# Kernel optimization log

Measured on AMD Instinct MI355X. Metric: run time of the kernel, lower is better.

The kernel has to match this reference:

```python
import jax, jax.numpy as jnp
import numpy as np
from jax import lax

B, CIN, COUT, H, W = 4, 256, 256, 64, 64
K = 3  # kernel size
PAD = 1
STRIDE = 1


def setup_inputs() -> dict:
    key = jax.random.key(0)
    k1, k2, k3, k4 = jax.random.split(key, 4)
    x = jax.random.normal(k1, (B, CIN, H, W), dtype=jnp.float32)
    # small offset weights so learned offsets are modest (original init is zeros)
    offset_w = jax.random.normal(k2, (3 * K * K, CIN, K, K), dtype=jnp.float32) * 0.01
    offset_b = jax.random.normal(k3, (3 * K * K,), dtype=jnp.float32) * 0.01
    dcn_w = jax.random.normal(k4, (COUT, CIN, K, K), dtype=jnp.float32) * (1.0 / np.sqrt(CIN * K * K))
    return {"x": x, "offset_w": offset_w, "offset_b": offset_b, "dcn_w": dcn_w}


def _dcnv2(x, offset_w, offset_b, dcn_w):
    b, c, h, w = x.shape
    kk = K * K
    # offset conv (standard 3x3, stride 1, pad 1)
    o = lax.conv_general_dilated(
        x, offset_w, (STRIDE, STRIDE), ((PAD, PAD), (PAD, PAD)),
        dimension_numbers=("NCHW", "OIHW", "NCHW"))
    o = o + offset_b[None, :, None, None]
    ho, wo = o.shape[2], o.shape[3]
    off = o[:, : 2 * kk].reshape(b, kk, 2, ho, wo)  # pairs are (dy, dx)
    dy, dx = off[:, :, 0], off[:, :, 1]             # [b,kk,ho,wo]
    mask = jax.nn.sigmoid(o[:, 2 * kk:])            # [b,kk,ho,wo]

    ki, kj = jnp.meshgrid(jnp.arange(K), jnp.arange(K), indexing="ij")
    ki = ki.reshape(kk).astype(jnp.float32)
    kj = kj.reshape(kk).astype(jnp.float32)
    base_y = (jnp.arange(ho, dtype=jnp.float32) * STRIDE - PAD)[None, None, :, None] + ki[None, :, None, None]
    base_x = (jnp.arange(wo, dtype=jnp.float32) * STRIDE - PAD)[None, None, None, :] + kj[None, :, None, None]
    py = base_y + dy  # [b,kk,ho,wo] sampling y
    px = base_x + dx  # sampling x

    y0 = jnp.floor(py)
    x0 = jnp.floor(px)
    wy = py - y0  # bilinear fractional weights
    wx = px - x0
    y0i = y0.astype(jnp.int32)
    x0i = x0.astype(jnp.int32)

    xT = x.transpose(0, 2, 3, 1)  # [b,h,w,c] for channel-last gathers
    bidx = jnp.arange(b)[:, None, None, None]

    def gather(yi, xi):
        # zero padding outside the image
        valid = (yi >= 0) & (yi < h) & (xi >= 0) & (xi < w)
        yc = jnp.clip(yi, 0, h - 1)
        xc = jnp.clip(xi, 0, w - 1)
        v = xT[bidx, yc, xc]  # [b,kk,ho,wo,c]
        return v * valid[..., None].astype(x.dtype)

    g00 = gather(y0i, x0i)
    g01 = gather(y0i, x0i + 1)
    g10 = gather(y0i + 1, x0i)
    g11 = gather(y0i + 1, x0i + 1)

    wy_ = wy[..., None]
    wx_ = wx[..., None]
    sampled = (g00 * (1 - wy_) * (1 - wx_) + g01 * (1 - wy_) * wx_
               + g10 * wy_ * (1 - wx_) + g11 * wy_ * wx_)
    sampled = sampled * mask[..., None]  # modulation

    wk = dcn_w.reshape(dcn_w.shape[0], c, kk)  # [o,c,kk]
    return jnp.einsum("bkhwc,ock->bohw", sampled, wk)


def reference(x, offset_w, offset_b, dcn_w):
    return _dcnv2(x, offset_w, offset_b, dcn_w)
```

## Files before the change

### kernel.cpp

```cpp
#include <hip/hip_runtime.h>
#include <hip/hip_bf16.h>
#include <stdint.h>
#include <math.h>

#define KDIM 2304

typedef __attribute__((ext_vector_type(8))) short bf16x8;
typedef __attribute__((ext_vector_type(4))) float f32x4;

__device__ inline unsigned short f2bf(float f) {
  union { float f; unsigned int u; } v; v.f = f;
  unsigned int u = v.u;
  unsigned int r = (u + 0x7FFFu + ((u >> 16) & 1u)) >> 16;
  return (unsigned short)r;
}
__device__ inline float bf2f(unsigned short h) {
  union { unsigned int u; float f; } v; v.u = ((unsigned int)h) << 16;
  return v.f;
}

__device__ inline void gl2lds16(const void* g, void* l) {
  __builtin_amdgcn_global_load_lds((const __attribute__((address_space(1))) void*)g,
                                   (__attribute__((address_space(3))) void*)l,
                                   16, 0, 0);
}

#define GLOAD16(dst, ptr) \
  asm volatile("global_load_dwordx4 %0, %1, off" : "=v"(dst) : "v"(ptr))

__global__ __launch_bounds__(256) void k_prep(const float* __restrict__ x,
                                              unsigned short* __restrict__ xTb,
                                              const float* __restrict__ dcn_w,
                                              const float* __restrict__ offset_w,
                                              unsigned short* __restrict__ Wpk,
                                              unsigned short* __restrict__ Wob,
                                              unsigned short* __restrict__ zp) {
  __shared__ float tile[32][65];
  int bx = (int)blockIdx.x;
  int t = threadIdx.x;
  if (bx < 2048) {
    int pt = bx & 127, ct = (bx >> 7) & 3, b = bx >> 9;
    int p0 = pt * 32, c0 = ct * 64;
    const float* xb = x + ((size_t)b << 20);
#pragma unroll
    for (int i = 0; i < 2; ++i) {
      int idx = t + i * 256;
      int c = idx >> 3, pq = idx & 7;
      float4 v = *(const float4*)(xb + ((size_t)(c0 + c) << 12) + p0 + pq * 4);
      tile[pq * 4 + 0][c] = v.x;
      tile[pq * 4 + 1][c] = v.y;
      tile[pq * 4 + 2][c] = v.z;
      tile[pq * 4 + 3][c] = v.w;
    }
    __syncthreads();
    unsigned short* ob = xTb + ((size_t)b << 20);
#pragma unroll
    for (int i = 0; i < 2; ++i) {
      int idx = t + i * 256;
      int p = idx >> 4, cg = idx & 15;
      ushort4 o;
      o.x = f2bf(tile[p][cg * 4 + 0]);
      o.y = f2bf(tile[p][cg * 4 + 1]);
      o.z = f2bf(tile[p][cg * 4 + 2]);
      o.w = f2bf(tile[p][cg * 4 + 3]);
      *(ushort4*)(ob + (((size_t)(p0 + p)) << 8) + c0 + cg * 4) = o;
    }
  } else {
    int gid = (bx - 2048) * 256 + t;
    const int N1 = 72 * 8192;
    const int N2 = 32 * KDIM;
    if (gid < N1) {
      int j = gid & 7;
      int lane = (gid >> 3) & 63;
      int mb = (gid >> 9) & 15;
      int kc = gid >> 13;
      int row = mb * 16 + (lane & 15);
      int gk = kc * 32 + ((lane >> 4) << 3) + j;
      int c = gk & 255, kidx = gk >> 8;
      Wpk[gid] = f2bf(dcn_w[((size_t)(row * 256 + c)) * 9 + kidx]);
    } else if (gid < N1 + N2) {
      int g = gid - N1;
      int ch = g / KDIM, k = g % KDIM;
      int kidx = k >> 8, c = k & 255;
      Wob[g] = (ch < 27) ? f2bf(offset_w[((size_t)(ch * 256 + c)) * 9 + kidx])
                         : (unsigned short)0;
    } else if (gid < N1 + N2 + 128) {
      zp[gid - N1 - N2] = 0;
    }
  }
}

__global__ __launch_bounds__(256) void k_offs(const unsigned short* __restrict__ xTb,
                                              const unsigned short* __restrict__ Wob,
                                              const unsigned short* __restrict__ zp,
                                              const float* __restrict__ offb,
                                              float* __restrict__ SW) {
  __shared__ unsigned short As[4][32 * 32];
  __shared__ unsigned short Bs[4][32 * 32];
  __shared__ float Os[32][33];
  int t = threadIdx.x;
  int wv = t >> 6, lane = t & 63;
  int bid = (int)blockIdx.x;
  int swz = (bid & 7) * 64 + (bid >> 3);
  int n0 = swz * 32;

  int r0 = (t >> 2) & 31, coff = (t & 3) * 8;
  int rowA = n0 + r0;
  int b_ = rowA >> 12, hw = rowA & 4095, h = hw >> 6, w = hw & 63;
  int rB = ((t - 128) >> 2) & 31;

  f32x4 acc = {};

  auto stage = [&](int kt) {
    int buf = kt & 3;
    int k0 = kt * 32;
    int kidx = k0 >> 8, c0 = k0 & 255;
    if (t < 128) {
      int di = kidx / 3 - 1, dj = kidx % 3 - 1;
      int y = h + di, xx = w + dj;
      const unsigned short* g = (y >= 0 && y < 64 && xx >= 0 && xx < 64)
          ? xTb + (((((size_t)b_) << 12) + (y << 6) + xx) << 8) + c0 + coff
          : zp;
      gl2lds16(g, (char*)As[buf] + wv * 1024);
    } else {
      const unsigned short* gB = Wob + (size_t)rB * KDIM + k0 + coff;
      gl2lds16(gB, (char*)Bs[buf] + (wv - 2) * 1024);
    }
  };

  stage(0); stage(1); stage(2);

  int mf = wv & 1, nf = wv >> 1;
  for (int kt = 0; kt < 72; ++kt) {
    if (kt <= 69)      asm volatile("s_waitcnt vmcnt(2)" ::: "memory");
    else if (kt == 70) asm volatile("s_waitcnt vmcnt(1)" ::: "memory");
    else               asm volatile("s_waitcnt vmcnt(0)" ::: "memory");
    asm volatile("s_barrier" ::: "memory");
    if (kt + 3 < 72) stage(kt + 3);
    int buf = kt & 3;
    bf16x8 aF = *(const bf16x8*)(As[buf] + (mf * 16 + (lane & 15)) * 32 + (lane >> 4) * 8);
    bf16x8 bF = *(const bf16x8*)(Bs[buf] + (nf * 16 + (lane & 15)) * 32 + (lane >> 4) * 8);
    acc = __builtin_amdgcn_mfma_f32_16x16x32_bf16(aF, bF, acc, 0, 0, 0);
  }

  int quad = lane >> 4, cl = lane & 15;
#pragma unroll
  for (int r = 0; r < 4; ++r)
    Os[mf * 16 + quad * 4 + r][nf * 16 + cl] = acc[r];
  __syncthreads();

  for (int item = t; item < 288; item += 256) {
    int bl = item & 31, k = item >> 5;
    int bhw = n0 + bl;
    int h_ = (bhw >> 6) & 63, w_ = bhw & 63;
    float dy = Os[bl][2 * k]     + offb[2 * k];
    float dx = Os[bl][2 * k + 1] + offb[2 * k + 1];
    float mv = Os[bl][18 + k]    + offb[18 + k];
    float mask = 1.0f / (1.0f + expf(-mv));

    float py = (float)(h_ - 1 + k / 3) + dy;
    float px = (float)(w_ - 1 + k % 3) + dx;
    float y0f = floorf(py), x0f = floorf(px);
    float wy = py - y0f, wx = px - x0f;
    int y0 = (int)y0f, x0 = (int)x0f;
    int y1 = y0 + 1, x1 = x0 + 1;

    float vy0 = (y0 >= 0 && y0 < 64) ? 1.f : 0.f;
    float vy1 = (y1 >= 0 && y1 < 64) ? 1.f : 0.f;
    float vx0 = (x0 >= 0 && x0 < 64) ? 1.f : 0.f;
    float vx1 = (x1 >= 0 && x1 < 64) ? 1.f : 0.f;
    int y0c = min(max(y0, 0), 63), y1c = min(max(y1, 0), 63);
    int x0c = min(max(x0, 0), 63), x1c = min(max(x1, 0), 63);

    float4 wv4;
    wv4.x = (1.f - wy) * (1.f - wx) * vy0 * vx0 * mask;
    wv4.y = (1.f - wy) * wx * vy0 * vx1 * mask;
    wv4.z = wy * (1.f - wx) * vy1 * vx0 * mask;
    wv4.w = wy * wx * vy1 * vx1 * mask;
    uint4 ov;
    ov.x = (unsigned)(((y0c << 6) + x0c) << 8);
    ov.y = (unsigned)(((y0c << 6) + x1c) << 8);
    ov.z = (unsigned)(((y1c << 6) + x0c) << 8);
    ov.w = (unsigned)(((y1c << 6) + x1c) << 8);

    float* p = SW + (size_t)(k * 16384 + bhw) * 8;
    *(float4*)p = wv4;
    *(uint4*)(p + 4) = ov;
  }
}

#define PHASE(PH, Q, AF, BUF, WB, WM)                                          \
  do {                                                                         \
    if (((PH) & 3) == 0) {                                                     \
      int g_ = (PH) >> 2;                                                      \
      wv4 = *(const float4*)(SWL + (size_t)(g_ * 128 + r * 2) * 4);            \
      ov  = *(const uint4*)(SWL + (size_t)(g_ * 128 + r * 2 + 1) * 4);         \
    } else if (((PH) & 3) == 2 && (PH) < 32) {                                 \
      ov  = *(const uint4*)(SWL + (size_t)((((PH) >> 2) + 1) * 128 + r * 2 + 1) * 4); \
    }                                                                          \
    asm volatile("s_waitcnt vmcnt(" #WB ")" ::: "memory");                     \
    __builtin_amdgcn_sched_barrier(0);                                         \
    float s_[8];                                                               \
    _Pragma("unroll")                                                          \
    for (int j_ = 0; j_ < 8; ++j_)                                             \
      s_[j_] = wv4.x * bf2f((unsigned short)Q[0][j_]) +                        \
               wv4.y * bf2f((unsigned short)Q[1][j_]) +                        \
               wv4.z * bf2f((unsigned short)Q[2][j_]) +                        \
               wv4.w * bf2f((unsigned short)Q[3][j_]);                         \
    union { __hip_bfloat162 h2[4]; bf16x8 v; } pk_;                            \
    pk_.h2[0] = __float22bfloat162_rn(make_float2(s_[0], s_[1]));              \
    pk_.h2[1] = __float22bfloat162_rn(make_float2(s_[2], s_[3]));              \
    pk_.h2[2] = __float22bfloat162_rn(make_float2(s_[4], s_[5]));              \
    pk_.h2[3] = __float22bfloat162_rn(make_float2(s_[6], s_[7]));              \
    *(bf16x8*)(&Bs[BUF][s_th][bsw]) = pk_.v;                                   \
    if ((PH) < 34) {                                                           \
      int kn0_ = 2 * (PH) + 4;                                                 \
      unsigned c_ = (unsigned)((((kn0_ & 7) + s_th) << 5) + gg * 8);           \
      GLOAD16(Q[0], xb + ov.x + c_);                                           \
      GLOAD16(Q[1], xb + ov.y + c_);                                           \
      GLOAD16(Q[2], xb + ov.z + c_);                                           \
      GLOAD16(Q[3], xb + ov.w + c_);                                           \
    }                                                                          \
    asm volatile("s_waitcnt vmcnt(" #WM ") lgkmcnt(0)\n\ts_barrier" ::: "memory"); \
    __builtin_amdgcn_sched_barrier(0);                                         \
    _Pragma("unroll")                                                          \
    for (int s2_ = 0; s2_ < 2; ++s2_) {                                        \
      bf16x8 bF0_ = *(const bf16x8*)(                                          \
          &Bs[BUF][s2_][(wn * 32 + (lane & 15)) * 56 + (lane >> 4) * 8]);      \
      bf16x8 bF1_ = *(const bf16x8*)(                                          \
          &Bs[BUF][s2_][(wn * 32 + 16 + (lane & 15)) * 56 + (lane >> 4) * 8]); \
      _Pragma("unroll")                                                        \
      for (int i_ = 0; i_ < 4; ++i_) {                                         \
        acc[i_][0] = __builtin_amdgcn_mfma_f32_16x16x32_bf16(                  \
            AF[s2_ * 4 + i_], bF0_, acc[i_][0], 0, 0, 0);                      \
        acc[i_][1] = __builtin_amdgcn_mfma_f32_16x16x32_bf16(                  \
            AF[s2_ * 4 + i_], bF1_, acc[i_][1], 0, 0, 0);                      \
      }                                                                        \
    }                                                                          \
    if ((PH) < 34) {                                                           \
      _Pragma("unroll")                                                        \
      for (int i_ = 0; i_ < 8; ++i_) {                                         \
        const unsigned short* ap_ =                                            \
            wpBase + ((size_t)((2 * (PH) + 4 + (i_ >> 2)) * 16 + (i_ & 3))) * 512; \
        GLOAD16(AF[i_], ap_);                                                  \
      }                                                                        \
    }                                                                          \
  } while (0)

__global__ __launch_bounds__(512, 2) void k_fused(const unsigned short* __restrict__ Wpk,
                                                  const unsigned short* __restrict__ xTb,
                                                  const float* __restrict__ SW,
                                                  float* __restrict__ out) {
  __shared__ __align__(16) unsigned short Bs[2][2][64 * 56];
  __shared__ __align__(16) float SWL[1152 * 4];
  int t = threadIdx.x;
  int wv = t >> 6, lane = t & 63;
  int wm = wv & 3, wn = wv >> 2;
  int bid = (int)blockIdx.x;
  int swz = (bid & 7) * 32 + (bid >> 3);
  int n0 = swz * 64;
  int b  = n0 >> 12;
  const unsigned short* xb = xTb + ((size_t)b << 20);

  int r = t >> 3;
  int u = t & 7;
  int s_th = u & 1, gg = u >> 1;
  int bsw = r * 56 + gg * 8;

  const unsigned short* wpBase = Wpk + ((size_t)(wm * 4 * 64 + lane)) * 8;

  f32x4 acc[4][2] = {};

  {
#pragma unroll
    for (int i = 0; i < 3; ++i) {
      int hs = t + i * 512;
      if (hs < 1152) {
        int grp = hs >> 7, row = (hs >> 1) & 63, hh = hs & 1;
        const float* src = SW + ((size_t)(grp * 16384 + n0 + row)) * 8 + hh * 4;
        char* dstbase = (char*)SWL + ((size_t)((t & ~63) + i * 512)) * 16;
        gl2lds16(src, dstbase);
      }
    }
  }
  asm volatile("s_waitcnt vmcnt(0)" ::: "memory");
  __builtin_amdgcn_s_barrier();

  float4 wv4; uint4 ov;
  wv4 = *(const float4*)(SWL + (size_t)(r * 2) * 4);
  ov  = *(const uint4*)(SWL + (size_t)(r * 2 + 1) * 4);

  bf16x8 qA[4], qB[4];
  bf16x8 aFA[8], aFB[8];

  {
    unsigned cA = (unsigned)((s_th << 5) + gg * 8);
    GLOAD16(qA[0], xb + ov.x + cA);
    GLOAD16(qA[1], xb + ov.y + cA);
    GLOAD16(qA[2], xb + ov.z + cA);
    GLOAD16(qA[3], xb + ov.w + cA);
#pragma unroll
    for (int i = 0; i < 8; ++i) {
      const unsigned short* ap = wpBase + ((size_t)(((i >> 2)) * 16 + (i & 3))) * 512;
      GLOAD16(aFA[i], ap);
    }
    unsigned cB = (unsigned)(((2 + s_th) << 5) + gg * 8);
    GLOAD16(qB[0], xb + ov.x + cB);
    GLOAD16(qB[1], xb + ov.y + cB);
    GLOAD16(qB[2], xb + ov.z + cB);
    GLOAD16(qB[3], xb + ov.w + cB);
#pragma unroll
    for (int i = 0; i < 8; ++i) {
      const unsigned short* ap = wpBase + ((size_t)((2 + (i >> 2)) * 16 + (i & 3))) * 512;
      GLOAD16(aFB[i], ap);
    }
  }

  for (int ph = 0; ph < 34; ph += 2) {
    PHASE(ph,     qA, aFA, 0, 20, 16);
    PHASE(ph + 1, qB, aFB, 1, 20, 16);
  }
  PHASE(34, qA, aFA, 0, 20, 12);
  PHASE(35, qB, aFB, 1, 8, 0);

  int quad = lane >> 4, cl = lane & 15;
  float* ob = out + (((size_t)b) << 20);
#pragma unroll
  for (int i = 0; i < 4; ++i) {
    int mbase = wm * 64 + i * 16 + quad * 4;
#pragma unroll
    for (int j = 0; j < 2; ++j) {
      int hw = (n0 & 4095) + wn * 32 + j * 16 + cl;
      float* op = ob + hw;
#pragma unroll
      for (int rr = 0; rr < 4; ++rr)
        op[((size_t)(mbase + rr)) << 12] = acc[i][j][rr];
    }
  }
}

extern "C" void kernel_launch(void* const* d_in, const int* in_sizes, int n_in,
                              void* d_out, int out_size, void* d_ws, size_t ws_size,
                              hipStream_t stream) {
  const float* x        = (const float*)d_in[0];
  const float* offset_w = (const float*)d_in[1];
  const float* offset_b = (const float*)d_in[2];
  const float* dcn_w    = (const float*)d_in[3];
  float* out = (float*)d_out;

  char* ws = (char*)d_ws;
  size_t off = 0;
  auto carve = [&](size_t bytes) -> void* {
    void* p = ws + off;
    off += (bytes + 255) & ~(size_t)255;
    return p;
  };
  unsigned short* xTb = (unsigned short*)carve(4ull * 64 * 64 * 256 * 2);
  unsigned short* Wpk = (unsigned short*)carve(72ull * 8192 * 2);
  unsigned short* Wob = (unsigned short*)carve(32ull * KDIM * 2);
  unsigned short* zp  = (unsigned short*)carve(256);
  float*          SW  = (float*)carve(9ull * 16384 * 8 * 4);
  (void)ws_size; (void)in_sizes; (void)n_in; (void)out_size;

  const int WPREP_BLOCKS = (72 * 8192 + 32 * KDIM + 128 + 255) / 256;
  k_prep<<<dim3(2048 + WPREP_BLOCKS), 256, 0, stream>>>(
      x, xTb, dcn_w, offset_w, Wpk, Wob, zp);
  k_offs<<<dim3(512), 256, 0, stream>>>(xTb, Wob, zp, offset_b, SW);
  k_fused<<<dim3(256), 512, 0, stream>>>(Wpk, xTb, SW, out);
}
```

Before: 131.6 us.

## Double fused-kernel block size to 1024 threads, halving per-thread gather and MFMA work

The fused deformable-conv GEMM kernel now launches 1024 threads per block instead of 512. Each thread gathers 4 channels with dwordx2 loads instead of 8 with dwordx4, and each wave keeps a 4x1 MFMA accumulator tile instead of 4x2. The aim is more waves to hide gather latency and fewer registers per thread. The cost is more block-wide barriers and halved reuse of each A fragment per wave, and the offset kernel also gains an extra barrier per k-step.

After: 158.1 us. 20.1% more time.

```diff
diff --git a/kernel.cpp b/kernel.cpp
--- a/kernel.cpp
+++ b/kernel.cpp
@@ -7,6 +7,7 @@
 
 typedef __attribute__((ext_vector_type(8))) short bf16x8;
 typedef __attribute__((ext_vector_type(4))) float f32x4;
+typedef __attribute__((ext_vector_type(2))) unsigned int u32x2;
 
 __device__ inline unsigned short f2bf(float f) {
   union { float f; unsigned int u; } v; v.f = f;
@@ -27,6 +28,8 @@
 
 #define GLOAD16(dst, ptr) \
   asm volatile("global_load_dwordx4 %0, %1, off" : "=v"(dst) : "v"(ptr))
+#define GLOAD8(dst, ptr) \
+  asm volatile("global_load_dwordx2 %0, %1, off" : "=v"(dst) : "v"(ptr))
 
 __global__ __launch_bounds__(256) void k_prep(const float* __restrict__ x,
                                               unsigned short* __restrict__ xTb,
@@ -96,7 +99,7 @@
                                               const float* __restrict__ offb,
                                               float* __restrict__ SW) {
   __shared__ unsigned short As[4][32 * 32];
-  __shared__ unsigned short Bs[4][32 * 32];
+  __shared__ unsigned short Bsf[4][32 * 32];
   __shared__ float Os[32][33];
   int t = threadIdx.x;
   int wv = t >> 6, lane = t & 63;
@@ -124,7 +127,7 @@
       gl2lds16(g, (char*)As[buf] + wv * 1024);
     } else {
       const unsigned short* gB = Wob + (size_t)rB * KDIM + k0 + coff;
-      gl2lds16(gB, (char*)Bs[buf] + (wv - 2) * 1024);
+      gl2lds16(gB, (char*)Bsf[buf] + (wv - 2) * 1024);
     }
   };
 
@@ -139,14 +142,16 @@
     if (kt + 3 < 72) stage(kt + 3);
     int buf = kt & 3;
     bf16x8 aF = *(const bf16x8*)(As[buf] + (mf * 16 + (lane & 15)) * 32 + (lane >> 4) * 8);
-    bf16x8 bF = *(const bf16x8*)(Bs[buf] + (nf * 16 + (lane & 15)) * 32 + (lane >> 4) * 8);
+    bf16x8 bF = *(const bf16x8*)(Bsf[buf] + (nf * 16 + (lane & 15)) * 32 + (lane >> 4) * 8);
     acc = __builtin_amdgcn_mfma_f32_16x16x32_bf16(aF, bF, acc, 0, 0, 0);
+
+    asm volatile("s_barrier" ::: "memory");
   }
 
   int quad = lane >> 4, cl = lane & 15;
 #pragma unroll
-  for (int r = 0; r < 4; ++r)
-    Os[mf * 16 + quad * 4 + r][nf * 16 + cl] = acc[r];
+  for (int rr = 0; rr < 4; ++rr)
+    Os[mf * 16 + quad * 4 + rr][nf * 16 + cl] = acc[rr];
   __syncthreads();
 
   for (int item = t; item < 288; item += 256) {
@@ -200,42 +205,38 @@
     }                                                                          \
     asm volatile("s_waitcnt vmcnt(" #WB ")" ::: "memory");                     \
     __builtin_amdgcn_sched_barrier(0);                                         \
-    float s_[8];                                                               \
-    _Pragma("unroll")                                                          \
-    for (int j_ = 0; j_ < 8; ++j_)                                             \
-      s_[j_] = wv4.x * bf2f((unsigned short)Q[0][j_]) +                        \
-               wv4.y * bf2f((unsigned short)Q[1][j_]) +                        \
-               wv4.z * bf2f((unsigned short)Q[2][j_]) +                        \
-               wv4.w * bf2f((unsigned short)Q[3][j_]);                         \
-    union { __hip_bfloat162 h2[4]; bf16x8 v; } pk_;                            \
-    pk_.h2[0] = __float22bfloat162_rn(make_float2(s_[0], s_[1]));              \
-    pk_.h2[1] = __float22bfloat162_rn(make_float2(s_[2], s_[3]));              \
-    pk_.h2[2] = __float22bfloat162_rn(make_float2(s_[4], s_[5]));              \
-    pk_.h2[3] = __float22bfloat162_rn(make_float2(s_[6], s_[7]));              \
-    *(bf16x8*)(&Bs[BUF][s_th][bsw]) = pk_.v;                                   \
+    {                                                                          \
+      union U_ { u32x2 d; unsigned short u[4]; };                              \
+      U_ q0_, q1_, q2_, q3_;                                                   \
+      q0_.d = Q[0]; q1_.d = Q[1]; q2_.d = Q[2]; q3_.d = Q[3];                  \
+      float s_[4];                                                             \
+      _Pragma("unroll")                                                        \
+      for (int j_ = 0; j_ < 4; ++j_)                                           \
+        s_[j_] = wv4.x * bf2f(q0_.u[j_]) + wv4.y * bf2f(q1_.u[j_]) +           \
+                 wv4.z * bf2f(q2_.u[j_]) + wv4.w * bf2f(q3_.u[j_]);            \
+      union { __hip_bfloat162 h2[2]; ushort4 v; } pk_;                         \
+      pk_.h2[0] = __float22bfloat162_rn(make_float2(s_[0], s_[1]));            \
+      pk_.h2[1] = __float22bfloat162_rn(make_float2(s_[2], s_[3]));            \
+      *(ushort4*)(&Bs[BUF][s_th][bsw]) = pk_.v;                                \
+    }                                                                          \
     if ((PH) < 34) {                                                           \
       int kn0_ = 2 * (PH) + 4;                                                 \
-      unsigned c_ = (unsigned)((((kn0_ & 7) + s_th) << 5) + gg * 8);           \
-      GLOAD16(Q[0], xb + ov.x + c_);                                           \
-      GLOAD16(Q[1], xb + ov.y + c_);                                           \
-      GLOAD16(Q[2], xb + ov.z + c_);                                           \
-      GLOAD16(Q[3], xb + ov.w + c_);                                           \
+      unsigned c_ = (unsigned)((((kn0_ & 7) + s_th) << 5) + gg * 4);           \
+      GLOAD8(Q[0], xb + ov.x + c_);                                            \
+      GLOAD8(Q[1], xb + ov.y + c_);                                            \
+      GLOAD8(Q[2], xb + ov.z + c_);                                            \
+      GLOAD8(Q[3], xb + ov.w + c_);                                            \
     }                                                                          \
     asm volatile("s_waitcnt vmcnt(" #WM ") lgkmcnt(0)\n\ts_barrier" ::: "memory"); \
     __builtin_amdgcn_sched_barrier(0);                                         \
     _Pragma("unroll")                                                          \
     for (int s2_ = 0; s2_ < 2; ++s2_) {                                        \
-      bf16x8 bF0_ = *(const bf16x8*)(                                          \
-          &Bs[BUF][s2_][(wn * 32 + (lane & 15)) * 56 + (lane >> 4) * 8]);      \
-      bf16x8 bF1_ = *(const bf16x8*)(                                          \
-          &Bs[BUF][s2_][(wn * 32 + 16 + (lane & 15)) * 56 + (lane >> 4) * 8]); \
+      bf16x8 bF_ = *(const bf16x8*)(                                           \
+          &Bs[BUF][s2_][(wn * 16 + (lane & 15)) * 56 + (lane >> 4) * 8]);      \
       _Pragma("unroll")                                                        \
-      for (int i_ = 0; i_ < 4; ++i_) {                                         \
-        acc[i_][0] = __builtin_amdgcn_mfma_f32_16x16x32_bf16(                  \
-            AF[s2_ * 4 + i_], bF0_, acc[i_][0], 0, 0, 0);                      \
-        acc[i_][1] = __builtin_amdgcn_mfma_f32_16x16x32_bf16(                  \
-            AF[s2_ * 4 + i_], bF1_, acc[i_][1], 0, 0, 0);                      \
-      }                                                                        \
+      for (int i_ = 0; i_ < 4; ++i_)                                           \
+        acc[i_] = __builtin_amdgcn_mfma_f32_16x16x32_bf16(                     \
+            AF[s2_ * 4 + i_], bF_, acc[i_], 0, 0, 0);                          \
     }                                                                          \
     if ((PH) < 34) {                                                           \
       _Pragma("unroll")                                                        \
@@ -247,10 +248,10 @@
     }                                                                          \
   } while (0)
 
-__global__ __launch_bounds__(512, 2) void k_fused(const unsigned short* __restrict__ Wpk,
-                                                  const unsigned short* __restrict__ xTb,
-                                                  const float* __restrict__ SW,
-                                                  float* __restrict__ out) {
+__global__ __launch_bounds__(1024, 2) void k_fused(const unsigned short* __restrict__ Wpk,
+                                                   const unsigned short* __restrict__ xTb,
+                                                   const float* __restrict__ SW,
+                                                   float* __restrict__ out) {
   __shared__ __align__(16) unsigned short Bs[2][2][64 * 56];
   __shared__ __align__(16) float SWL[1152 * 4];
   int t = threadIdx.x;
@@ -262,23 +263,23 @@
   int b  = n0 >> 12;
   const unsigned short* xb = xTb + ((size_t)b << 20);
 
-  int r = t >> 3;
-  int u = t & 7;
+  int r = t >> 4;
+  int u = t & 15;
   int s_th = u & 1, gg = u >> 1;
-  int bsw = r * 56 + gg * 8;
+  int bsw = r * 56 + gg * 4;
 
   const unsigned short* wpBase = Wpk + ((size_t)(wm * 4 * 64 + lane)) * 8;
 
-  f32x4 acc[4][2] = {};
+  f32x4 acc[4] = {};
 
   {
 #pragma unroll
-    for (int i = 0; i < 3; ++i) {
-      int hs = t + i * 512;
+    for (int i = 0; i < 2; ++i) {
+      int hs = t + i * 1024;
       if (hs < 1152) {
         int grp = hs >> 7, row = (hs >> 1) & 63, hh = hs & 1;
         const float* src = SW + ((size_t)(grp * 16384 + n0 + row)) * 8 + hh * 4;
-        char* dstbase = (char*)SWL + ((size_t)((t & ~63) + i * 512)) * 16;
+        char* dstbase = (char*)SWL + ((size_t)((t & ~63) + i * 1024)) * 16;
         gl2lds16(src, dstbase);
       }
     }
@@ -290,25 +291,25 @@
   wv4 = *(const float4*)(SWL + (size_t)(r * 2) * 4);
   ov  = *(const uint4*)(SWL + (size_t)(r * 2 + 1) * 4);
 
-  bf16x8 qA[4], qB[4];
+  u32x2 qA[4], qB[4];
   bf16x8 aFA[8], aFB[8];
 
   {
-    unsigned cA = (unsigned)((s_th << 5) + gg * 8);
-    GLOAD16(qA[0], xb + ov.x + cA);
-    GLOAD16(qA[1], xb + ov.y + cA);
-    GLOAD16(qA[2], xb + ov.z + cA);
-    GLOAD16(qA[3], xb + ov.w + cA);
+    unsigned cA = (unsigned)((s_th << 5) + gg * 4);
+    GLOAD8(qA[0], xb + ov.x + cA);
+    GLOAD8(qA[1], xb + ov.y + cA);
+    GLOAD8(qA[2], xb + ov.z + cA);
+    GLOAD8(qA[3], xb + ov.w + cA);
 #pragma unroll
     for (int i = 0; i < 8; ++i) {
       const unsigned short* ap = wpBase + ((size_t)(((i >> 2)) * 16 + (i & 3))) * 512;
       GLOAD16(aFA[i], ap);
     }
-    unsigned cB = (unsigned)(((2 + s_th) << 5) + gg * 8);
-    GLOAD16(qB[0], xb + ov.x + cB);
-    GLOAD16(qB[1], xb + ov.y + cB);
-    GLOAD16(qB[2], xb + ov.z + cB);
-    GLOAD16(qB[3], xb + ov.w + cB);
+    unsigned cB = (unsigned)(((2 + s_th) << 5) + gg * 4);
+    GLOAD8(qB[0], xb + ov.x + cB);
+    GLOAD8(qB[1], xb + ov.y + cB);
+    GLOAD8(qB[2], xb + ov.z + cB);
+    GLOAD8(qB[3], xb + ov.w + cB);
 #pragma unroll
     for (int i = 0; i < 8; ++i) {
       const unsigned short* ap = wpBase + ((size_t)((2 + (i >> 2)) * 16 + (i & 3))) * 512;
@@ -328,14 +329,11 @@
 #pragma unroll
   for (int i = 0; i < 4; ++i) {
     int mbase = wm * 64 + i * 16 + quad * 4;
-#pragma unroll
-    for (int j = 0; j < 2; ++j) {
-      int hw = (n0 & 4095) + wn * 32 + j * 16 + cl;
-      float* op = ob + hw;
-#pragma unroll
-      for (int rr = 0; rr < 4; ++rr)
-        op[((size_t)(mbase + rr)) << 12] = acc[i][j][rr];
-    }
+    int hw = (n0 & 4095) + wn * 16 + cl;
+    float* op = ob + hw;
+#pragma unroll
+    for (int rr = 0; rr < 4; ++rr)
+      op[((size_t)(mbase + rr)) << 12] = acc[i][rr];
   }
 }
 
@@ -366,5 +364,5 @@
   k_prep<<<dim3(2048 + WPREP_BLOCKS), 256, 0, stream>>>(
       x, xTb, dcn_w, offset_w, Wpk, Wob, zp);
   k_offs<<<dim3(512), 256, 0, stream>>>(xTb, Wob, zp, offset_b, SW);
-  k_fused<<<dim3(256), 512, 0, stream>>>(Wpk, xTb, SW, out);
-}
+  k_fused<<<dim3(256), 1024, 0, stream>>>(Wpk, xTb, SW, out);
+}
```
